# Optimization experiments

Hardware: AMD Instinct MI355X
Metric: run time of the kernel (lower is better)

## Reference

```python
import jax, jax.numpy as jnp
import numpy as np

B, N, E, K, DI, DO = 16, 1024, 16, 3, 32, 32


def setup_inputs() -> dict:
    key = jax.random.key(0)
    k1, k2, k3, k4, k5 = jax.random.split(key, 5)
    return {
        "x": jax.random.normal(k1, (B, N, DI), dtype=jnp.float32),
        "all_emb": jax.random.normal(k2, (B, N, E), dtype=jnp.float32),
        "stock_emb": jax.random.normal(k3, (B, N, E), dtype=jnp.float32),
        "weights_pool": jax.random.normal(k4, (E, K, DI, DO), dtype=jnp.float32) * 0.1,
        "bias_pool": jax.random.normal(k5, (E, DO), dtype=jnp.float32) * 0.1,
    }


def reference(x, all_emb, stock_emb, weights_pool, bias_pool):
    # dynamic adjacency: relu(E E^T) then row softmax -> [B, N, N]
    A = jax.nn.relu(jnp.einsum('bne,bme->bnm', all_emb, all_emb))
    S = jax.nn.softmax(A, axis=-1)
    b, n, _ = S.shape
    k_orders = weights_pool.shape[1]
    eye = jnp.broadcast_to(jnp.eye(n, dtype=S.dtype), S.shape)
    # Chebyshev recursion T_0 = I, T_1 = S, T_k = 2 S T_{k-1} - T_{k-2}
    supports = [eye, S]
    for _ in range(2, k_orders):
        supports.append(2.0 * jnp.matmul(S, supports[-1]) - supports[-2])
    cheby = jnp.stack(supports, axis=1)  # [B, K, N, N]
    # graph propagation per Chebyshev order: [B, K, N, dim_in]
    x_g = jnp.einsum('bkij,bjd->bkid', cheby, x)
    # node-specific weights from stock_emb, fused with conv (avoids [B,N,K,I,O]):
    # original: weights = einsum('bni,ikop->bnkop'); out = einsum('bkni,bnkio->bnko').sum(k)
    out = jnp.einsum('bkni,bne,ekio->bno', x_g, stock_emb, weights_pool)
    bias = jnp.einsum('bne,eo->bno', stock_emb, bias_pool)
    return out + bias
```

## Files before the change

kernel.cpp:

```cpp
#include <hip/hip_runtime.h>
#include <stdint.h>

typedef __bf16 bf16x8 __attribute__((ext_vector_type(8)));
typedef __bf16 bf16x4 __attribute__((ext_vector_type(4)));
typedef float  f32x16 __attribute__((ext_vector_type(16)));

constexpr int kB = 16;
constexpr int kN = 1024;
constexpr float kLog2e = 1.44269504088896340736f;

struct bfhl { __bf16 h, l; };
__device__ __forceinline__ bfhl hilo(float v) {
    bfhl r;
    r.h = (__bf16)v;
    r.l = (__bf16)(v - (float)r.h);
    return r;
}

__device__ __forceinline__ int moff(int f, int h, int j) {
    return 16 * f + ((j < 4) ? (4 * h + j) : (4 * h + j + 4));
}

template<int STAGE>
__global__ __launch_bounds__(256, 2) void apply_mfma(
    const float* __restrict__ emb, const float* __restrict__ x,
    const float* __restrict__ Wp,
    const float* __restrict__ stock, const float* __restrict__ bias,
    const __bf16* __restrict__ vtin,
    __bf16* __restrict__ vtout,
    __bf16* __restrict__ y1f,
    __bf16* __restrict__ wq,
    float* __restrict__ out)
{
    __shared__ alignas(16) char smem[28672];
    float*  ps  = (float*)smem;
    float*  Ls  = (float*)(smem + 16896);
    float*  yb  = (float*)(smem + 17408);
    __bf16* xg2 = (__bf16*)(smem + 22016);
    float*  s_s = (float*)(smem + 26624);

    const int tid = threadIdx.x;
    const int w = tid >> 6, l = tid & 63;
    const int q = l & 31, h = l >> 5;
    const int bs = ((blockIdx.x & 7) << 6) | (blockIdx.x >> 3);
    const int b = bs >> 5, nt = bs & 31, q0 = nt << 5;
    const int gnt = b * 32 + nt;

    const float* embB = emb + (size_t)b * kN * 16;
    const float* xB   = x + (size_t)b * kN * 32;
    const __bf16* vtinB = vtin + (size_t)b * 32768;

    if (STAGE == 1) {
        if (blockIdx.x < 48 && tid < 128) {
            int idx = blockIdx.x * 128 + tid;
            int e = idx / 384, rem = idx - e * 384;
            int ks = rem / 64, r2 = rem - ks * 64;
            int o = r2 >> 1, hh = r2 & 1;
            int ki0 = ks * 16 + hh * 8;
            bf16x8 hi;
            #pragma unroll
            for (int j = 0; j < 8; ++j)
                hi[j] = (__bf16)Wp[(size_t)e * 3072 + (size_t)(ki0 + j) * 32 + o];
            *(bf16x8*)(wq + (size_t)(e * 6 + ks) * 512 + o * 16 + hh * 8) = hi;
        }
    }
    if (STAGE == 2) {
        int r = tid >> 3, e2 = (tid & 7) * 2;
        *(float2*)(s_s + r * 16 + e2) =
            *(const float2*)(stock + (size_t)(b * kN + q0 + r) * 16 + e2);
    }

    bf16x8 bhi, blo;
    {
        const float* ep = embB + (size_t)(q0 + q) * 16 + 8 * h;
        float4 u0 = *(const float4*)ep;
        float4 u1 = *(const float4*)(ep + 4);
        float u[8] = {u0.x, u0.y, u0.z, u0.w, u1.x, u1.y, u1.z, u1.w};
        #pragma unroll
        for (int j = 0; j < 8; ++j) {
            bfhl t = hilo(u[j] * kLog2e);
            bhi[j] = t.h; blo[j] = t.l;
        }
    }

    f32x16 acc = {};
    float Lp = 0.f;

#define LOADE(kt_, e0_, e1_) {                                            \
    const float* ep_ = embB + (size_t)((kt_) * 32 + q) * 16 + 8 * h;      \
    e0_ = *(const float4*)ep_; e1_ = *(const float4*)(ep_ + 4); }
#define LOADV1(kt_, vv_) {                                                \
    _Pragma("unroll")                                                     \
    for (int j_ = 0; j_ < 8; ++j_) {                                      \
        vv_[j_]     = xB[(size_t)((kt_) * 32 + moff(0, h, j_)) * 32 + q]; \
        vv_[8 + j_] = xB[(size_t)((kt_) * 32 + moff(1, h, j_)) * 32 + q]; } }
#define LOADV2(kt_, A0_, A1_) {                                           \
    A0_ = *(const bf16x8*)(vtinB + ((size_t)(kt_) * 2) * 512 + l * 8);    \
    A1_ = *(const bf16x8*)(vtinB + ((size_t)(kt_) * 2 + 1) * 512 + l * 8); }

    {
        const int ktb = w * 8;
        float4 e0c, e1c, e0n, e1n;
        float vc[16], vn[16];
        bf16x8 A0c, A1c, A0n, A1n;

        LOADE(ktb, e0c, e1c);
        if (STAGE == 1) { LOADV1(ktb, vc) } else { LOADV2(ktb, A0c, A1c) }

        #pragma unroll
        for (int it = 0; it < 8; ++it) {
            if (it < 7) {
                LOADE(ktb + it + 1, e0n, e1n);
                if (STAGE == 1) { LOADV1(ktb + it + 1, vn) }
                else            { LOADV2(ktb + it + 1, A0n, A1n) }
            }
            float ef[8] = {e0c.x, e0c.y, e0c.z, e0c.w, e1c.x, e1c.y, e1c.z, e1c.w};
            bf16x8 ahi, alo;
            #pragma unroll
            for (int j = 0; j < 8; ++j) {
                bfhl t = hilo(ef[j]);
                ahi[j] = t.h; alo[j] = t.l;
            }
            bf16x8 A0, A1;
            if (STAGE == 1) {
                #pragma unroll
                for (int j = 0; j < 8; ++j) {
                    A0[j] = (__bf16)vc[j];
                    A1[j] = (__bf16)vc[8 + j];
                }
            } else { A0 = A0c; A1 = A1c; }

            __builtin_amdgcn_s_setprio(1);
            f32x16 S = {};
            S = __builtin_amdgcn_mfma_f32_32x32x16_bf16(ahi, bhi, S, 0, 0, 0);
            S = __builtin_amdgcn_mfma_f32_32x32x16_bf16(ahi, blo, S, 0, 0, 0);
            S = __builtin_amdgcn_mfma_f32_32x32x16_bf16(alo, bhi, S, 0, 0, 0);
            __builtin_amdgcn_s_setprio(0);

            float p[16];
            #pragma unroll
            for (int r = 0; r < 16; ++r) {
                p[r] = exp2f(fmaxf(S[r], 0.f));
                Lp += p[r];
            }
            bf16x8 P0, P1;
            #pragma unroll
            for (int j = 0; j < 8; ++j) { P0[j] = (__bf16)p[j]; P1[j] = (__bf16)p[8 + j]; }

            __builtin_amdgcn_s_setprio(1);
            acc = __builtin_amdgcn_mfma_f32_32x32x16_bf16(A0, P0, acc, 0, 0, 0);
            acc = __builtin_amdgcn_mfma_f32_32x32x16_bf16(A1, P1, acc, 0, 0, 0);
            __builtin_amdgcn_s_setprio(0);

            e0c = e0n; e1c = e1n;
            if (STAGE == 1) {
                #pragma unroll
                for (int j = 0; j < 16; ++j) vc[j] = vn[j];
            } else { A0c = A0n; A1c = A1n; }
        }
    }
#undef LOADE
#undef LOADV1
#undef LOADV2

    Lp += __shfl_xor(Lp, 32);
    #pragma unroll
    for (int r = 0; r < 16; ++r) {
        int d = (r & 3) + 8 * (r >> 2) + 4 * h;
        ps[w * 1056 + d * 33 + q] = acc[r];
    }
    if (l < 32) Ls[w * 32 + l] = Lp;
    __syncthreads();

    const int qq = tid >> 3, dg = tid & 7;
    const float iL = 1.f / (Ls[qq] + Ls[32 + qq] + Ls[64 + qq] + Ls[96 + qq]);
    float yv[4];
    #pragma unroll
    for (int i = 0; i < 4; ++i) {
        int d = dg * 4 + i;
        yv[i] = (ps[d * 33 + qq] + ps[1056 + d * 33 + qq] +
                 ps[2112 + d * 33 + qq] + ps[3168 + d * 33 + qq]) * iL;
    }

    if (STAGE == 1) {
        #pragma unroll
        for (int i = 0; i < 4; ++i) yb[qq * 36 + dg * 4 + i] = yv[i];
        __syncthreads();
        if (tid < 128) {
            int fr = tid >> 6, l2 = tid & 63;
            int d = l2 & 31, h2 = l2 >> 5;
            bf16x8 ov;
            #pragma unroll
            for (int j = 0; j < 8; ++j)
                ov[j] = (__bf16)yb[moff(fr, h2, j) * 36 + d];
            *(bf16x8*)(vtout + ((size_t)gnt * 2 + fr) * 512 + l2 * 8) = ov;
        }
        {
            int ks2 = tid >> 7, pl = (tid >> 6) & 1, l2 = tid & 63;
            int node = l2 & 31, h2 = l2 >> 5;
            const float* rp = yb + node * 36 + ks2 * 16 + 8 * h2;
            bf16x8 ov;
            #pragma unroll
            for (int j = 0; j < 8; ++j) {
                bfhl tt = hilo(rp[j]);
                ov[j] = pl ? tt.l : tt.h;
            }
            *(bf16x8*)(y1f + (((size_t)gnt * 2 + ks2) * 2 + pl) * 512 + l2 * 8) = ov;
        }
    } else {
        {
            float4 xv = *(const float4*)(xB + (size_t)(q0 + qq) * 32 + dg * 4);
            float xa[4] = {xv.x, xv.y, xv.z, xv.w};
            bf16x4 hi, lo;
            #pragma unroll
            for (int i = 0; i < 4; ++i) {
                bfhl tt = hilo(2.f * yv[i] - xa[i]);
                hi[i] = tt.h; lo[i] = tt.l;
            }
            *(bf16x4*)(xg2 + qq * 36 + dg * 4)        = hi;
            *(bf16x4*)(xg2 + 1152 + qq * 36 + dg * 4) = lo;
        }
        __syncthreads();

        f32x16 acc2[4] = {};
        const int e0 = w * 4;
        const int o = q;

        #pragma unroll
        for (int ks = 0; ks < 6; ++ks) {
            bf16x8 Ah, Al;
            if (ks < 2) {
                const float* rp = xB + (size_t)(q0 + q) * 32 + ks * 16 + 8 * h;
                float4 u0 = *(const float4*)rp;
                float4 u1 = *(const float4*)(rp + 4);
                float u[8] = {u0.x, u0.y, u0.z, u0.w, u1.x, u1.y, u1.z, u1.w};
                #pragma unroll
                for (int j = 0; j < 8; ++j) { bfhl tt = hilo(u[j]); Ah[j] = tt.h; Al[j] = tt.l; }
            } else if (ks < 4) {
                Ah = *(const bf16x8*)(y1f + (((size_t)gnt * 2 + (ks - 2)) * 2 + 0) * 512 + l * 8);
                Al = *(const bf16x8*)(y1f + (((size_t)gnt * 2 + (ks - 2)) * 2 + 1) * 512 + l * 8);
            } else {
                const int base = o * 36 + (ks - 4) * 16 + 8 * h;
                bf16x4 a0 = *(const bf16x4*)(xg2 + base);
                bf16x4 a1 = *(const bf16x4*)(xg2 + base + 4);
                bf16x4 b0 = *(const bf16x4*)(xg2 + 1152 + base);
                bf16x4 b1 = *(const bf16x4*)(xg2 + 1152 + base + 4);
                #pragma unroll
                for (int j = 0; j < 4; ++j) {
                    Ah[j] = a0[j]; Ah[4 + j] = a1[j];
                    Al[j] = b0[j]; Al[4 + j] = b1[j];
                }
            }
            #pragma unroll
            for (int ei = 0; ei < 4; ++ei) {
                bf16x8 Bh = *(const bf16x8*)(wq + (size_t)((e0 + ei) * 6 + ks) * 512 + o * 16 + h * 8);
                acc2[ei] = __builtin_amdgcn_mfma_f32_32x32x16_bf16(Ah, Bh, acc2[ei], 0, 0, 0);
                acc2[ei] = __builtin_amdgcn_mfma_f32_32x32x16_bf16(Al, Bh, acc2[ei], 0, 0, 0);
            }
        }

        float pr[16];
        #pragma unroll
        for (int r = 0; r < 16; ++r) pr[r] = 0.f;
        #pragma unroll
        for (int ei = 0; ei < 4; ++ei) {
            const int eg = e0 + ei;
            const float bv = bias[eg * 32 + o];
            #pragma unroll
            for (int r = 0; r < 16; ++r) {
                int node = (r & 3) + 8 * (r >> 2) + 4 * h;
                pr[r] += s_s[node * 16 + eg] * (acc2[ei][r] + bv);
            }
        }
        #pragma unroll
        for (int r = 0; r < 16; ++r) {
            int node = (r & 3) + 8 * (r >> 2) + 4 * h;
            ps[w * 1056 + node * 33 + o] = pr[r];
        }
        __syncthreads();
        {
            const int node = tid >> 3, og = (tid & 7) * 4;
            float4 s;
            #pragma unroll
            for (int i = 0; i < 4; ++i) {
                int c = node * 33 + og + i;
                ((float*)&s)[i] = ps[c] + ps[1056 + c] + ps[2112 + c] + ps[3168 + c];
            }
            *(float4*)(out + (size_t)(b * kN + q0 + node) * 32 + og) = s;
        }
    }
}

extern "C" void kernel_launch(void* const* d_in, const int* in_sizes, int n_in,
                              void* d_out, int out_size, void* d_ws, size_t ws_size,
                              hipStream_t stream) {
    const float* x     = (const float*)d_in[0];
    const float* aemb  = (const float*)d_in[1];
    const float* stock = (const float*)d_in[2];
    const float* Wp    = (const float*)d_in[3];
    const float* bias  = (const float*)d_in[4];
    float* out = (float*)d_out;

    __bf16* wsb  = (__bf16*)d_ws;
    __bf16* vtf2 = wsb;
    __bf16* y1f  = wsb + 524288;
    __bf16* wq   = wsb + 1572864;

    apply_mfma<1><<<dim3(512), dim3(256), 0, stream>>>(
        aemb, x, Wp, stock, bias, nullptr, vtf2, y1f, wq, out);
    apply_mfma<2><<<dim3(512), dim3(256), 0, stream>>>(
        aemb, x, Wp, stock, bias, vtf2, nullptr, y1f, wq, out);
}
```

Baseline: 29.00 us.

## Use eight waves per block and drop manual software prefetch

Blocks grow from 256 to 512 threads, so each wave handles 4 key tiles instead of 8, and the cross-wave reduction runs over 8 partial sums. The stage-2 expert loop is split across 8 waves with 2 experts each. The explicit double-buffered register prefetch is removed, which lowers register pressure to allow 4 waves per SIMD in exchange for relying on the scheduler to hide latency. LDS use grows for the larger partial-sum buffer, and yb now aliases xg2.

```diff
diff --git a/kernel.cpp b/kernel.cpp
--- a/kernel.cpp
+++ b/kernel.cpp
@@ -3,6 +3,7 @@
 
 typedef __bf16 bf16x8 __attribute__((ext_vector_type(8)));
 typedef __bf16 bf16x4 __attribute__((ext_vector_type(4)));
+typedef __bf16 bf16x2 __attribute__((ext_vector_type(2)));
 typedef float  f32x16 __attribute__((ext_vector_type(16)));
 
 constexpr int kB = 16;
@@ -22,7 +23,7 @@
 }
 
 template<int STAGE>
-__global__ __launch_bounds__(256, 2) void apply_mfma(
+__global__ __launch_bounds__(512, 4) void apply_mfma(
     const float* __restrict__ emb, const float* __restrict__ x,
     const float* __restrict__ Wp,
     const float* __restrict__ stock, const float* __restrict__ bias,
@@ -32,12 +33,12 @@
     __bf16* __restrict__ wq,
     float* __restrict__ out)
 {
-    __shared__ alignas(16) char smem[28672];
+    __shared__ alignas(16) char smem[41472];
     float*  ps  = (float*)smem;
-    float*  Ls  = (float*)(smem + 16896);
-    float*  yb  = (float*)(smem + 17408);
-    __bf16* xg2 = (__bf16*)(smem + 22016);
-    float*  s_s = (float*)(smem + 26624);
+    float*  Ls  = (float*)(smem + 33792);
+    float*  yb  = (float*)(smem + 34816);
+    __bf16* xg2 = (__bf16*)(smem + 34816);
+    float*  s_s = (float*)(smem + 39424);
 
     const int tid = threadIdx.x;
     const int w = tid >> 6, l = tid & 63;
@@ -65,9 +66,11 @@
         }
     }
     if (STAGE == 2) {
-        int r = tid >> 3, e2 = (tid & 7) * 2;
-        *(float2*)(s_s + r * 16 + e2) =
-            *(const float2*)(stock + (size_t)(b * kN + q0 + r) * 16 + e2);
+        if (tid < 256) {
+            int r = tid >> 3, e2 = (tid & 7) * 2;
+            *(float2*)(s_s + r * 16 + e2) =
+                *(const float2*)(stock + (size_t)(b * kN + q0 + r) * 16 + e2);
+        }
     }
 
     bf16x8 bhi, blo;
@@ -86,49 +89,34 @@
     f32x16 acc = {};
     float Lp = 0.f;
 
-#define LOADE(kt_, e0_, e1_) {                                            \
-    const float* ep_ = embB + (size_t)((kt_) * 32 + q) * 16 + 8 * h;      \
-    e0_ = *(const float4*)ep_; e1_ = *(const float4*)(ep_ + 4); }
-#define LOADV1(kt_, vv_) {                                                \
-    _Pragma("unroll")                                                     \
-    for (int j_ = 0; j_ < 8; ++j_) {                                      \
-        vv_[j_]     = xB[(size_t)((kt_) * 32 + moff(0, h, j_)) * 32 + q]; \
-        vv_[8 + j_] = xB[(size_t)((kt_) * 32 + moff(1, h, j_)) * 32 + q]; } }
-#define LOADV2(kt_, A0_, A1_) {                                           \
-    A0_ = *(const bf16x8*)(vtinB + ((size_t)(kt_) * 2) * 512 + l * 8);    \
-    A1_ = *(const bf16x8*)(vtinB + ((size_t)(kt_) * 2 + 1) * 512 + l * 8); }
-
     {
-        const int ktb = w * 8;
-        float4 e0c, e1c, e0n, e1n;
-        float vc[16], vn[16];
-        bf16x8 A0c, A1c, A0n, A1n;
-
-        LOADE(ktb, e0c, e1c);
-        if (STAGE == 1) { LOADV1(ktb, vc) } else { LOADV2(ktb, A0c, A1c) }
-
-        #pragma unroll
-        for (int it = 0; it < 8; ++it) {
-            if (it < 7) {
-                LOADE(ktb + it + 1, e0n, e1n);
-                if (STAGE == 1) { LOADV1(ktb + it + 1, vn) }
-                else            { LOADV2(ktb + it + 1, A0n, A1n) }
-            }
-            float ef[8] = {e0c.x, e0c.y, e0c.z, e0c.w, e1c.x, e1c.y, e1c.z, e1c.w};
+        const int ktb = w * 4;
+        #pragma unroll
+        for (int it = 0; it < 4; ++it) {
+            const int kt = ktb + it;
             bf16x8 ahi, alo;
-            #pragma unroll
-            for (int j = 0; j < 8; ++j) {
-                bfhl t = hilo(ef[j]);
-                ahi[j] = t.h; alo[j] = t.l;
+            {
+                const float* ep = embB + (size_t)(kt * 32 + q) * 16 + 8 * h;
+                float4 u0 = *(const float4*)ep;
+                float4 u1 = *(const float4*)(ep + 4);
+                float u[8] = {u0.x, u0.y, u0.z, u0.w, u1.x, u1.y, u1.z, u1.w};
+                #pragma unroll
+                for (int j = 0; j < 8; ++j) {
+                    bfhl t = hilo(u[j]);
+                    ahi[j] = t.h; alo[j] = t.l;
+                }
             }
             bf16x8 A0, A1;
             if (STAGE == 1) {
                 #pragma unroll
                 for (int j = 0; j < 8; ++j) {
-                    A0[j] = (__bf16)vc[j];
-                    A1[j] = (__bf16)vc[8 + j];
+                    A0[j] = (__bf16)xB[(size_t)(kt * 32 + moff(0, h, j)) * 32 + q];
+                    A1[j] = (__bf16)xB[(size_t)(kt * 32 + moff(1, h, j)) * 32 + q];
                 }
-            } else { A0 = A0c; A1 = A1c; }
+            } else {
+                A0 = *(const bf16x8*)(vtinB + ((size_t)kt * 2) * 512 + l * 8);
+                A1 = *(const bf16x8*)(vtinB + ((size_t)kt * 2 + 1) * 512 + l * 8);
+            }
 
             __builtin_amdgcn_s_setprio(1);
             f32x16 S = {};
@@ -151,17 +139,8 @@
             acc = __builtin_amdgcn_mfma_f32_32x32x16_bf16(A0, P0, acc, 0, 0, 0);
             acc = __builtin_amdgcn_mfma_f32_32x32x16_bf16(A1, P1, acc, 0, 0, 0);
             __builtin_amdgcn_s_setprio(0);
-
-            e0c = e0n; e1c = e1n;
-            if (STAGE == 1) {
-                #pragma unroll
-                for (int j = 0; j < 16; ++j) vc[j] = vn[j];
-            } else { A0c = A0n; A1c = A1n; }
-        }
-    }
-#undef LOADE
-#undef LOADV1
-#undef LOADV2
+        }
+    }
 
     Lp += __shfl_xor(Lp, 32);
     #pragma unroll
@@ -172,19 +151,25 @@
     if (l < 32) Ls[w * 32 + l] = Lp;
     __syncthreads();
 
-    const int qq = tid >> 3, dg = tid & 7;
-    const float iL = 1.f / (Ls[qq] + Ls[32 + qq] + Ls[64 + qq] + Ls[96 + qq]);
-    float yv[4];
-    #pragma unroll
-    for (int i = 0; i < 4; ++i) {
-        int d = dg * 4 + i;
-        yv[i] = (ps[d * 33 + qq] + ps[1056 + d * 33 + qq] +
-                 ps[2112 + d * 33 + qq] + ps[3168 + d * 33 + qq]) * iL;
+    const int qq = tid >> 4, dgi = tid & 15;
+    float yv[2];
+    {
+        float Lsum = 0.f;
+        #pragma unroll
+        for (int k = 0; k < 8; ++k) Lsum += Ls[k * 32 + qq];
+        const float iL = 1.f / Lsum;
+        #pragma unroll
+        for (int i = 0; i < 2; ++i) {
+            int d = dgi * 2 + i;
+            float s = 0.f;
+            #pragma unroll
+            for (int k = 0; k < 8; ++k) s += ps[k * 1056 + d * 33 + qq];
+            yv[i] = s * iL;
+        }
     }
 
     if (STAGE == 1) {
-        #pragma unroll
-        for (int i = 0; i < 4; ++i) yb[qq * 36 + dg * 4 + i] = yv[i];
+        *(float2*)(yb + qq * 36 + dgi * 2) = make_float2(yv[0], yv[1]);
         __syncthreads();
         if (tid < 128) {
             int fr = tid >> 6, l2 = tid & 63;
@@ -195,7 +180,7 @@
                 ov[j] = (__bf16)yb[moff(fr, h2, j) * 36 + d];
             *(bf16x8*)(vtout + ((size_t)gnt * 2 + fr) * 512 + l2 * 8) = ov;
         }
-        {
+        if (tid < 256) {
             int ks2 = tid >> 7, pl = (tid >> 6) & 1, l2 = tid & 63;
             int node = l2 & 31, h2 = l2 >> 5;
             const float* rp = yb + node * 36 + ks2 * 16 + 8 * h2;
@@ -209,21 +194,19 @@
         }
     } else {
         {
-            float4 xv = *(const float4*)(xB + (size_t)(q0 + qq) * 32 + dg * 4);
-            float xa[4] = {xv.x, xv.y, xv.z, xv.w};
-            bf16x4 hi, lo;
-            #pragma unroll
-            for (int i = 0; i < 4; ++i) {
-                bfhl tt = hilo(2.f * yv[i] - xa[i]);
-                hi[i] = tt.h; lo[i] = tt.l;
-            }
-            *(bf16x4*)(xg2 + qq * 36 + dg * 4)        = hi;
-            *(bf16x4*)(xg2 + 1152 + qq * 36 + dg * 4) = lo;
+            float2 xv = *(const float2*)(xB + (size_t)(q0 + qq) * 32 + dgi * 2);
+            bfhl t0 = hilo(2.f * yv[0] - xv.x);
+            bfhl t1 = hilo(2.f * yv[1] - xv.y);
+            bf16x2 hi2, lo2;
+            hi2[0] = t0.h; hi2[1] = t1.h;
+            lo2[0] = t0.l; lo2[1] = t1.l;
+            *(bf16x2*)(xg2 + qq * 36 + dgi * 2)        = hi2;
+            *(bf16x2*)(xg2 + 1152 + qq * 36 + dgi * 2) = lo2;
         }
         __syncthreads();
 
-        f32x16 acc2[4] = {};
-        const int e0 = w * 4;
+        f32x16 acc2[2] = {};
+        const int e0 = w * 2;
         const int o = q;
 
         #pragma unroll
@@ -252,7 +235,7 @@
                 }
             }
             #pragma unroll
-            for (int ei = 0; ei < 4; ++ei) {
+            for (int ei = 0; ei < 2; ++ei) {
                 bf16x8 Bh = *(const bf16x8*)(wq + (size_t)((e0 + ei) * 6 + ks) * 512 + o * 16 + h * 8);
                 acc2[ei] = __builtin_amdgcn_mfma_f32_32x32x16_bf16(Ah, Bh, acc2[ei], 0, 0, 0);
                 acc2[ei] = __builtin_amdgcn_mfma_f32_32x32x16_bf16(Al, Bh, acc2[ei], 0, 0, 0);
@@ -263,7 +246,7 @@
         #pragma unroll
         for (int r = 0; r < 16; ++r) pr[r] = 0.f;
         #pragma unroll
-        for (int ei = 0; ei < 4; ++ei) {
+        for (int ei = 0; ei < 2; ++ei) {
             const int eg = e0 + ei;
             const float bv = bias[eg * 32 + o];
             #pragma unroll
@@ -279,14 +262,15 @@
         }
         __syncthreads();
         {
-            const int node = tid >> 3, og = (tid & 7) * 4;
-            float4 s;
-            #pragma unroll
-            for (int i = 0; i < 4; ++i) {
-                int c = node * 33 + og + i;
-                ((float*)&s)[i] = ps[c] + ps[1056 + c] + ps[2112 + c] + ps[3168 + c];
-            }
-            *(float4*)(out + (size_t)(b * kN + q0 + node) * 32 + og) = s;
+            const int node = tid >> 4, og = (tid & 15) * 2;
+            float2 s = make_float2(0.f, 0.f);
+            #pragma unroll
+            for (int k = 0; k < 8; ++k) {
+                int c = k * 1056 + node * 33 + og;
+                s.x += ps[c];
+                s.y += ps[c + 1];
+            }
+            *(float2*)(out + (size_t)(b * kN + q0 + node) * 32 + og) = s;
         }
     }
 }
@@ -306,8 +290,8 @@
     __bf16* y1f  = wsb + 524288;
     __bf16* wq   = wsb + 1572864;
 
-    apply_mfma<1><<<dim3(512), dim3(256), 0, stream>>>(
+    apply_mfma<1><<<dim3(512), dim3(512), 0, stream>>>(
         aemb, x, Wp, stock, bias, nullptr, vtf2, y1f, wq, out);
-    apply_mfma<2><<<dim3(512), dim3(256), 0, stream>>>(
+    apply_mfma<2><<<dim3(512), dim3(512), 0, stream>>>(
         aemb, x, Wp, stock, bias, vtf2, nullptr, y1f, wq, out);
 }
```

Result: no change. 28.86 us (-0.5%).
